# Performance work log

Hardware: AMD Instinct MI355X
Metric: run time of the kernel (lower is better)

Reference implementation:

```python
import jax, jax.numpy as jnp
import numpy as np

V, H, B, T, L, G = 32000, 256, 16, 128, 50, 8
BETA, GAMMA = 5.0, 2.0
ATOL = 1e-8  # torch.allclose(x, zeros) default atol (rtol term vanishes vs zero)


def setup_inputs() -> dict:
    key = jax.random.key(0)
    ks = jax.random.split(key, 17)
    u = 1.0 / np.sqrt(H)
    def U(k, shape):
        return jax.random.uniform(k, shape, jnp.float32, -u, u)
    return dict(
        recipe=jax.random.randint(ks[0], (B, T), 0, V),
        g=jax.random.randint(ks[1], (B, G), 0, V),
        ingr=jax.random.randint(ks[2], (B, L), 0, V),
        wv=jax.random.normal(ks[3], (V, H), jnp.float32) * 0.1,  # frozen word vectors
        w_ih=U(ks[4], (5 * H, H)),
        w_hh=U(ks[5], (5 * H, H)),
        b_ih=U(ks[6], (5 * H,)),
        b_hh=U(ks[7], (5 * H,)),
        Z=U(ks[8], (H, H)),
        Y=U(ks[9], (H, H)),
        U_g=U(ks[10], (H, H)),
        z_bias=U(ks[11], (H,)),
        y_bias=U(ks[12], (H,)),
        S=U(ks[13], (3, H)),
        P=U(ks[14], (H, H)),
        fcW=U(ks[15], (V, H)),
        fcb=U(ks[16], (V,)),
    )


def _cgru_forward(x, g_vec, E, w_ih, w_hh, b_ih, b_hh, Z, Y, U_g, z_bias, y_bias, S, P):
    # x: (B,T,H) batch_first; g_vec: (B,H); E: (B,L,H)
    ht0 = g_vec @ U_g.T                      # init_hidden
    a0 = jnp.zeros((x.shape[0], E.shape[1]), x.dtype)
    E0 = E                                   # (1-a)*E with a=0
    ot0 = jnp.zeros_like(x[:, 0])
    goal_term = g_vec @ Y.T + y_bias         # constant across steps

    def step(carry, x_t):
        ht, ot, a, E_new = carry
        is_zero = jnp.all(jnp.abs(x_t) <= ATOL)
        # --- cell ---
        gi = x_t @ w_ih.T + b_ih
        gh = ht @ w_hh.T + b_hh
        i_r, i_u, i_n, i_g, i_i = jnp.split(gi, 5, axis=1)
        h_r, h_u, h_n, h_g, h_i = jnp.split(gh, 5, axis=1)
        z_t = jax.nn.sigmoid(i_u + h_u)
        r_t = jax.nn.sigmoid(i_r + h_r)
        s_t = jax.nn.sigmoid(i_g + h_g)
        q_t = jax.nn.sigmoid(i_i + h_i)
        tmp = E_new.sum(axis=1)              # 'mlk -> mk'
        h_tilde = jnp.tanh(i_n + r_t * h_n + s_t * goal_term + q_t * (tmp @ Z.T + z_bias))
        ht2 = h_tilde + z_t * (ht - h_tilde)
        # --- attention read/write ---
        ref = jax.nn.softmax((BETA * ht2) @ S.T, axis=-1)   # (B,3)
        h_proj = ht2 @ P.T
        En = (1.0 - a)[:, :, None] * E
        alpha_n = jax.nn.softmax(GAMMA * jnp.einsum('mk,mlk->ml', h_proj, En), axis=-1)
        c_n = jnp.einsum('mlk,ml->mk', E, alpha_n)
        Eu = a[:, :, None] * E
        alpha_u = jax.nn.softmax(GAMMA * jnp.einsum('mk,mlk->ml', h_proj, Eu), axis=-1)
        c_u = jnp.einsum('mlk,ml->mk', E, alpha_u)
        out = ref[:, 0:1] * h_proj + ref[:, 1:2] * c_n + ref[:, 2:3] * c_u
        a2 = a + ref[:, 1:2] * alpha_n
        # skip update when input step is all-zero (faithful to torch.allclose guard)
        ht_o = jnp.where(is_zero, ht, ht2)
        ot_o = jnp.where(is_zero, ot, out)
        a_o = jnp.where(is_zero, a, a2)
        E_o = jnp.where(is_zero, E_new, En)
        return (ht_o, ot_o, a_o, E_o), ot_o

    (ht, ot, a, E_new), outs = jax.lax.scan(step, (ht0, ot0, a0, E0),
                                            jnp.transpose(x, (1, 0, 2)))
    output = jnp.transpose(outs, (1, 0, 2))  # back to batch_first (B,T,H)
    return output, ht, a, E_new


def reference(recipe, g, ingr, wv, w_ih, w_hh, b_ih, b_hh, Z, Y, U_g,
              z_bias, y_bias, S, P, fcW, fcb):
    recipe_embed = wv[recipe]           # (B,T,H)
    goal_embed = wv[g].sum(axis=1)      # (B,H)
    E = wv[ingr]                        # (B,L,H)
    output, ht, a, E_new = _cgru_forward(recipe_embed, goal_embed, E,
                                         w_ih, w_hh, b_ih, b_hh, Z, Y, U_g,
                                         z_bias, y_bias, S, P)
    logits = output @ fcW.T + fcb       # (B,T,V)
    return logits, ht, a, E_new
```

## Files before the change

### kernel.cpp

```cpp
#include <hip/hip_runtime.h>

#define Hd   256
#define Bd   16
#define Td   128
#define Ld   50
#define Vd   32000
#define G5H  1280

typedef __attribute__((ext_vector_type(8))) short short8v;
typedef __attribute__((ext_vector_type(4))) float f32x4;

__device__ __forceinline__ unsigned short f2bu(float f) {
  unsigned u = __float_as_uint(f);
  unsigned r = (u + 0x7fffu + ((u >> 16) & 1u)) >> 16;
  return (unsigned short)r;
}
__device__ __forceinline__ float bu2f(unsigned short b) {
  return __uint_as_float(((unsigned)b) << 16);
}
__device__ __forceinline__ float sigm(float x) { return 1.f / (1.f + __expf(-x)); }

__device__ __forceinline__ void st_devu(unsigned* p, unsigned v) {
  __hip_atomic_store(p, v, __ATOMIC_RELAXED, __HIP_MEMORY_SCOPE_AGENT);
}
__device__ __forceinline__ unsigned ld_devu(const unsigned* p) {
  return __hip_atomic_load((unsigned*)p, __ATOMIC_RELAXED, __HIP_MEMORY_SCOPE_AGENT);
}
__device__ __forceinline__ void st_devd(double* p, double v) {
  __hip_atomic_store(p, v, __ATOMIC_RELAXED, __HIP_MEMORY_SCOPE_AGENT);
}
__device__ __forceinline__ double ld_devd(const double* p) {
  return __hip_atomic_load((double*)p, __ATOMIC_RELAXED, __HIP_MEMORY_SCOPE_AGENT);
}
__device__ __forceinline__ double pk2(float a, float b) {
  union { double d; float2 f; } u; u.f = make_float2(a, b); return u.d;
}

__global__ __launch_bounds__(256) void conv_kernel(
    const float* __restrict__ wv, const float* __restrict__ w_ih,
    const float* __restrict__ fcW, const float* __restrict__ w_hh,
    const float* __restrict__ Zm, const float* __restrict__ Pm,
    unsigned short* __restrict__ wv_b, unsigned short* __restrict__ wih_b,
    unsigned short* __restrict__ fcw_b, unsigned short* __restrict__ whh_f,
    unsigned short* __restrict__ z_f, unsigned short* __restrict__ p_f)
{
  const long N0 = 2048000, N1 = N0 + 81920, N2 = N1 + 2048000;
  const long NW = 81920, NZ = 16384, NP = 16384;
  const long N5 = N2 + NW + NZ + NP;
  for (long idx = (long)blockIdx.x * blockDim.x + threadIdx.x; idx < N5;
       idx += (long)gridDim.x * blockDim.x) {
    if (idx < N2) {
      const float* src; unsigned short* dst; long off;
      if      (idx < N0) { src = wv;   dst = wv_b;  off = idx; }
      else if (idx < N1) { src = w_ih; dst = wih_b; off = idx - N0; }
      else               { src = fcW;  dst = fcw_b; off = idx - N1; }
      float4 v = *(const float4*)(src + off * 4);
      ushort4 o;
      o.x = f2bu(v.x); o.y = f2bu(v.y); o.z = f2bu(v.z); o.w = f2bu(v.w);
      *(ushort4*)(dst + off * 4) = o;
    } else {
      long u = idx - N2;
      const float* src; unsigned short* dst;
      if      (u < NW)      { src = w_hh; dst = whh_f; }
      else if (u < NW + NZ) { src = Zm;   dst = z_f;  u -= NW; }
      else                  { src = Pm;   dst = p_f;  u -= NW + NZ; }
      long frag = u >> 7;
      int g128 = (int)(u & 127);
      int lane = g128 >> 1, e0 = (g128 & 1) * 4;
      long T = frag >> 3; int ks = (int)(frag & 7);
      int lr = lane & 15, lg = lane >> 4;
      float4 v = *(const float4*)(src + (T * 16 + lr) * 256 + ks * 32 + lg * 8 + e0);
      ushort4 o;
      o.x = f2bu(v.x); o.y = f2bu(v.y); o.z = f2bu(v.z); o.w = f2bu(v.w);
      *(ushort4*)(dst + u * 4) = o;
    }
  }
}

__global__ __launch_bounds__(256) void prep_kernel(
    const int* __restrict__ g, const int* __restrict__ ingr,
    const float* __restrict__ wv, const float* __restrict__ Ug,
    const float* __restrict__ Ym, const float* __restrict__ yb,
    float* __restrict__ E_ws, float* __restrict__ sumE,
    float* __restrict__ goal_ws, float* __restrict__ HT0)
{
  __shared__ float ge[256];
  const int b = blockIdx.x, tid = threadIdx.x;
  float s = 0.f;
  for (int i = 0; i < 8; ++i) s += wv[((size_t)g[(b << 3) + i] << 8) + tid];
  ge[tid] = s;
  __syncthreads();
  float h0 = 0.f, gt = 0.f;
  const float* ur = Ug + (tid << 8);
  const float* yr = Ym + (tid << 8);
#pragma unroll 8
  for (int k = 0; k < Hd; k += 4) {
    float4 gv = *(const float4*)(ge + k);
    float4 uv = *(const float4*)(ur + k);
    float4 yv = *(const float4*)(yr + k);
    h0 = fmaf(gv.x, uv.x, h0); h0 = fmaf(gv.y, uv.y, h0);
    h0 = fmaf(gv.z, uv.z, h0); h0 = fmaf(gv.w, uv.w, h0);
    gt = fmaf(gv.x, yv.x, gt); gt = fmaf(gv.y, yv.y, gt);
    gt = fmaf(gv.z, yv.z, gt); gt = fmaf(gv.w, yv.w, gt);
  }
  HT0[(b << 8) + tid] = h0;
  goal_ws[(b << 8) + tid] = gt + yb[tid];
  float se = 0.f;
  for (int l = 0; l < Ld; ++l) {
    float v = wv[((size_t)ingr[b * Ld + l] << 8) + tid];
    E_ws[((size_t)(b * Ld + l) << 8) + tid] = v;
    se += v;
  }
  sumE[(b << 8) + tid] = se;
}

template <int MODE>
__global__ __launch_bounds__(256) void gemm_bf16(
    const unsigned short* __restrict__ A, const unsigned short* __restrict__ Bmat,
    const int* __restrict__ ridx, const float* __restrict__ bias,
    float* __restrict__ C)
{
  __shared__ unsigned short As[128 * 64];
  __shared__ unsigned short Bs[128 * 64];
  const int tid = threadIdx.x;
  const int m0 = blockIdx.x << 7, n0 = blockIdx.y << 7;
  const int wave = tid >> 6, lane = tid & 63;
  const int wm = wave >> 1, wn = wave & 1;
  const int lr = lane & 15, lg = lane >> 4;

  f32x4 acc[4][4];
#pragma unroll
  for (int i = 0; i < 4; ++i)
#pragma unroll
    for (int jj = 0; jj < 4; ++jj) acc[i][jj] = (f32x4){0.f, 0.f, 0.f, 0.f};

  const int srow = tid >> 1, shalf = tid & 1;
  const unsigned short* arow;
  {
    int gm = m0 + srow;
    if (MODE == 0) {
      int tt = gm >> 4, bb = gm & 15;
      arow = A + (size_t)ridx[bb * Td + tt] * Hd;
    } else {
      arow = A + (size_t)gm * Hd;
    }
  }
  const unsigned short* brow = Bmat + (size_t)(n0 + srow) * Hd;

  for (int k0 = 0; k0 < Hd; k0 += 64) {
#pragma unroll
    for (int c = 0; c < 4; ++c) {
      int k = shalf * 32 + c * 8;
      uint4 va = *(const uint4*)(arow + k0 + k);
      uint4 vb = *(const uint4*)(brow + k0 + k);
      int byo = (srow << 7) + ((k << 1) ^ ((srow & 7) << 4));
      *(uint4*)((char*)As + byo) = va;
      *(uint4*)((char*)Bs + byo) = vb;
    }
    __syncthreads();
#pragma unroll
    for (int kk = 0; kk < 2; ++kk) {
      short8v af[4], bfr[4];
      const int kb = kk * 32 + lg * 8;
#pragma unroll
      for (int i = 0; i < 4; ++i) {
        int ar = wm * 64 + i * 16 + lr;
        af[i] = *(const short8v*)((const char*)As + (ar << 7) + ((kb << 1) ^ ((ar & 7) << 4)));
        int br = wn * 64 + i * 16 + lr;
        bfr[i] = *(const short8v*)((const char*)Bs + (br << 7) + ((kb << 1) ^ ((br & 7) << 4)));
      }
#pragma unroll
      for (int i = 0; i < 4; ++i)
#pragma unroll
        for (int jj = 0; jj < 4; ++jj)
          acc[i][jj] = __builtin_amdgcn_mfma_f32_16x16x32_bf16(af[i], bfr[jj], acc[i][jj], 0, 0, 0);
    }
    __syncthreads();
  }
#pragma unroll
  for (int i = 0; i < 4; ++i)
#pragma unroll
    for (int jj = 0; jj < 4; ++jj) {
      int col = n0 + wn * 64 + jj * 16 + lr;
      float bv = bias[col];
#pragma unroll
      for (int r = 0; r < 4; ++r) {
        int row = m0 + wm * 64 + i * 16 + lg * 4 + r;
        float v = acc[i][jj][r] + bv;
        if (MODE == 0) {
          int tt = row >> 4, bb = row & 15;
          C[((size_t)(bb * Td + tt)) * G5H + col] = v;
        } else {
          C[(size_t)row * Vd + col] = v;
        }
      }
    }
}

#define RNN_SMEM 150080
__global__ __launch_bounds__(512, 1) void rnn_kernel(
    const unsigned short* __restrict__ whh_f, const unsigned short* __restrict__ z_f,
    const unsigned short* __restrict__ p_f, const float* __restrict__ b_hh,
    const float* __restrict__ Sm, const float* __restrict__ z_bias,
    const float* __restrict__ gi, const float* __restrict__ goal_ws,
    const float* __restrict__ E_ws, const float* __restrict__ sumE,
    const float* __restrict__ HT0,
    unsigned short* __restrict__ out_all, float* __restrict__ d_out,
    double* __restrict__ XH, double* __restrict__ XP, unsigned* __restrict__ FL)
{
  extern __shared__ char smem[];
  unsigned short* w_lds = (unsigned short*)(smem);
  unsigned short* z_lds = (unsigned short*)(smem + 81920);
  unsigned short* p_lds = (unsigned short*)(smem + 98304);
  unsigned short* E_lds = (unsigned short*)(smem + 114688);
  float* hp    = (float*)(smem + 141088);
  float* gh_l  = (float*)(smem + 142112);
  float* zd    = (float*)(smem + 142752);
  float* se    = (float*)(smem + 142880);
  float* gl    = (float*)(smem + 143904);
  float* bh    = (float*)(smem + 144032);
  float* zb    = (float*)(smem + 144672);
  float* Sl    = (float*)(smem + 144800);
  float* a_l   = (float*)(smem + 145184);
  float* d_l   = (float*)(smem + 145440);
  float* an_l  = (float*)(smem + 145696);
  float* au_l  = (float*)(smem + 145952);
  float* sd    = (float*)(smem + 146208);
  float* refl  = (float*)(smem + 146224);
  unsigned short* tp_hi = (unsigned short*)(smem + 146240);
  unsigned short* tp_lo = (unsigned short*)(smem + 146752);
  unsigned short* hs_hi = (unsigned short*)(smem + 147264);
  unsigned short* hs_lo = (unsigned short*)(smem + 147328);
  float* hrow  = (float*)(smem + 147392);
  unsigned short* ht_hi = (unsigned short*)(smem + 148416);
  unsigned short* ht_lo = (unsigned short*)(smem + 148928);
  float* gi_l  = (float*)(smem + 149440);

  const int b  = blockIdx.x >> 3;
  const int j  = blockIdx.x & 7;
  const int hc0 = j << 5;
  const int tid = threadIdx.x;
  const int lane = tid & 63, wid = tid >> 6;
  const int lr = lane & 15, lg = lane >> 4;
  unsigned* FLb = FL + (b << 5);

  for (int idx = tid; idx < 5120; idx += 512) {
    int f = idx >> 6, e = idx & 63;
    int q = f >> 3, ks = f & 7;
    int T = (q >> 1) * 16 + 2 * j + (q & 1);
    *(uint4*)(w_lds + ((size_t)f << 9) + e * 8) =
        *(const uint4*)(whh_f + (((size_t)T * 8 + ks) << 9) + e * 8);
  }
  for (int idx = tid; idx < 1024; idx += 512) {
    int f = idx >> 6, e = idx & 63;
    int T = 2 * j + (f >> 3), ks = f & 7;
    *(uint4*)(z_lds + ((size_t)f << 9) + e * 8) =
        *(const uint4*)(z_f + (((size_t)T * 8 + ks) << 9) + e * 8);
  }
  for (int idx = tid; idx < 1024; idx += 512) {
    int f = idx >> 6, e = idx & 63;
    *(uint4*)(p_lds + ((size_t)f << 9) + e * 8) =
        *(const uint4*)(p_f + (((size_t)f * 8 + j) << 9) + e * 8);
  }
  for (int idx = tid; idx < Ld * 256; idx += 512) {
    int l = idx >> 8, k = idx & 255;
    E_lds[l * 264 + (k >> 5) * 33 + (k & 31)] =
        f2bu(E_ws[((size_t)(b * Ld + l) << 8) + k]);
  }
  if (tid < 160) bh[tid] = b_hh[((tid >> 5) << 8) + hc0 + (tid & 31)];
  if (tid < 96) Sl[tid] = Sm[((tid >> 5) << 8) + hc0 + (tid & 31)];
  if (tid < 32) {
    gl[tid] = goal_ws[(b << 8) + hc0 + tid];
    zb[tid] = z_bias[hc0 + tid];
  }
  if (tid < 256) {
    float s0 = sumE[(b << 8) + tid];
    se[tid] = s0;
    unsigned short hi = f2bu(s0);
    tp_hi[tid] = hi; tp_lo[tid] = f2bu(s0 - bu2f(hi));
    float h0 = HT0[(b << 8) + tid];
    hrow[tid] = h0;
    unsigned short hh = f2bu(h0);
    ht_hi[tid] = hh; ht_lo[tid] = f2bu(h0 - bu2f(hh));
  }
  if (tid < 64) a_l[tid] = 0.f;
  __syncthreads();

  if (wid < 4) {
#pragma unroll
    for (int i = 0; i < 3; ++i) {
      int q = wid + 4 * i;
      if (q < 10) {
        f32x4 acc = (f32x4){0.f, 0.f, 0.f, 0.f};
#pragma unroll
        for (int ks = 0; ks < 8; ++ks) {
          short8v av = *(const short8v*)(w_lds + ((size_t)(q * 8 + ks) << 9) + (lane << 3));
          short8v bv = (short8v){0,0,0,0,0,0,0,0};
          if (lr < 2)
            bv = *(const short8v*)((lr == 0 ? ht_hi : ht_lo) + ks * 32 + (lg << 3));
          acc = __builtin_amdgcn_mfma_f32_16x16x32_bf16(av, bv, acc, 0, 0, 0);
        }
#pragma unroll
        for (int r = 0; r < 4; ++r) {
          float v = acc[r] + __shfl_xor(acc[r], 1);
          if (lr == 0) gh_l[q * 16 + lg * 4 + r] = v;
        }
      }
    }
  } else if (wid == 4 || wid == 5) {
    int tz = wid - 4;
    f32x4 acc = (f32x4){0.f, 0.f, 0.f, 0.f};
#pragma unroll
    for (int ks = 0; ks < 8; ++ks) {
      short8v av = *(const short8v*)(z_lds + ((size_t)(tz * 8 + ks) << 9) + (lane << 3));
      short8v bv = (short8v){0,0,0,0,0,0,0,0};
      if (lr < 2)
        bv = *(const short8v*)((lr == 0 ? tp_hi : tp_lo) + ks * 32 + (lg << 3));
      acc = __builtin_amdgcn_mfma_f32_16x16x32_bf16(av, bv, acc, 0, 0, 0);
    }
#pragma unroll
    for (int r = 0; r < 4; ++r) {
      float v = acc[r] + __shfl_xor(acc[r], 1);
      if (lr == 0) zd[tz * 16 + lg * 4 + r] = v;
    }
  }
  __syncthreads();
  {
    double* XHp = XH + ((size_t)((0 * 16 + b) * 8 + j)) * 16;
    double* XPp = XP + ((size_t)((0 * 16 + b) * 8 + j)) * 132;
    if (tid < 32) {
      int cl = tid;
      const float* gib = gi + ((size_t)(b * Td)) * G5H + hc0 + cl;
      float g_ir = gib[0], g_iu = gib[256], g_in = gib[512];
      float g_ig = gib[768], g_ii = gib[1024];
      float hr = gh_l[cl]       + bh[cl];
      float hu = gh_l[32 + cl]  + bh[32 + cl];
      float hn = gh_l[64 + cl]  + bh[64 + cl];
      float hg = gh_l[96 + cl]  + bh[96 + cl];
      float hq = gh_l[128 + cl] + bh[128 + cl];
      float rt = sigm(g_ir + hr), zt = sigm(g_iu + hu);
      float st = sigm(g_ig + hg), qt = sigm(g_ii + hq);
      float htl = tanhf(g_in + rt * hn + st * gl[cl] + qt * (zd[cl] + zb[cl]));
      float h2 = htl + zt * (hrow[hc0 + cl] - htl);
      unsigned short hi = f2bu(h2);
      hs_hi[cl] = hi; hs_lo[cl] = f2bu(h2 - bu2f(hi));
      float h2o = __shfl_xor(h2, 1);
      if (!(cl & 1)) st_devd(XHp + (cl >> 1), pk2(h2, h2o));
      float p0 = Sl[cl] * h2, p1 = Sl[32 + cl] * h2, p2 = Sl[64 + cl] * h2;
      p0 += __shfl_xor(p0, 1);  p0 += __shfl_xor(p0, 2);  p0 += __shfl_xor(p0, 4);
      p0 += __shfl_xor(p0, 8);  p0 += __shfl_xor(p0, 16);
      p1 += __shfl_xor(p1, 1);  p1 += __shfl_xor(p1, 2);  p1 += __shfl_xor(p1, 4);
      p1 += __shfl_xor(p1, 8);  p1 += __shfl_xor(p1, 16);
      p2 += __shfl_xor(p2, 1);  p2 += __shfl_xor(p2, 2);  p2 += __shfl_xor(p2, 4);
      p2 += __shfl_xor(p2, 8);  p2 += __shfl_xor(p2, 16);
      if (cl == 0) {
        st_devd(XPp + 128, pk2(p0, p1));
        st_devd(XPp + 129, pk2(p2, 0.f));
      }
    }
    __syncthreads();
#pragma unroll
    for (int qq = 0; qq < 2; ++qq) {
      int q = wid * 2 + qq;
      short8v av = *(const short8v*)(p_lds + ((size_t)q << 9) + (lane << 3));
      short8v bv = (short8v){0,0,0,0,0,0,0,0};
      if (lr < 2)
        bv = *(const short8v*)((lr == 0 ? hs_hi : hs_lo) + (lg << 3));
      f32x4 acc = (f32x4){0.f, 0.f, 0.f, 0.f};
      acc = __builtin_amdgcn_mfma_f32_16x16x32_bf16(av, bv, acc, 0, 0, 0);
      float v0 = acc[0] + __shfl_xor(acc[0], 1);
      float v1 = acc[1] + __shfl_xor(acc[1], 1);
      float v2 = acc[2] + __shfl_xor(acc[2], 1);
      float v3 = acc[3] + __shfl_xor(acc[3], 1);
      if (lr == 0) {
        st_devd(XPp + q * 8 + lg * 2, pk2(v0, v1));
        st_devd(XPp + q * 8 + lg * 2 + 1, pk2(v2, v3));
      }
    }
    asm volatile("s_waitcnt vmcnt(0)" ::: "memory");
    __syncthreads();
    if (tid < 4) st_devu(FLb + j * 4 + tid, 1u);
  }

  for (int t = 0; t < Td; ++t) {
    const int par = t & 1, par1 = (t + 1) & 1;
    const double* XPr = XP + ((size_t)((par * 16 + b) * 8)) * 132;
    const double* XHr = XH + ((size_t)((par * 16 + b) * 8)) * 16;
    double* XPp = XP + ((size_t)((par1 * 16 + b) * 8 + j)) * 132;
    double* XHp = XH + ((size_t)((par1 * 16 + b) * 8 + j)) * 16;
    if (tid < 256) {
      int k = tid;
      int kp = (k >> 5) * 33 + (k & 31);
      float acct = 0.f;
#pragma unroll 10
      for (int l = 0; l < Ld; ++l)
        acct = fmaf(a_l[l], bu2f(E_lds[l * 264 + kp]), acct);
      float tn = se[k] - acct;
      unsigned short th = f2bu(tn);
      tp_hi[k] = th; tp_lo[k] = f2bu(tn - bu2f(th));
    } else {
      unsigned tgt = (unsigned)(t + 1);
      int guard = 0;
      while (1) {
        unsigned v = (lane < 32) ? ld_devu(FLb + lane) : tgt;
        if (__all((int)(v >= tgt))) break;
        __builtin_amdgcn_s_sleep(1);
        if (++guard > (1 << 20)) break;
      }
      int u = tid - 256;
      if (u < 128) {
        float2 f0, f1, f2, f3, f4, f5, f6, f7;
        { union { double d; float2 f; } u_;
          u_.d = ld_devd(XPr + 0 * 132 + u); f0 = u_.f;
          u_.d = ld_devd(XPr + 1 * 132 + u); f1 = u_.f;
          u_.d = ld_devd(XPr + 2 * 132 + u); f2 = u_.f;
          u_.d = ld_devd(XPr + 3 * 132 + u); f3 = u_.f;
          u_.d = ld_devd(XPr + 4 * 132 + u); f4 = u_.f;
          u_.d = ld_devd(XPr + 5 * 132 + u); f5 = u_.f;
          u_.d = ld_devd(XPr + 6 * 132 + u); f6 = u_.f;
          u_.d = ld_devd(XPr + 7 * 132 + u); f7 = u_.f; }
        hp[2 * u] =
          ((((((f0.x + f1.x) + f2.x) + f3.x) + f4.x) + f5.x) + f6.x) + f7.x;
        hp[2 * u + 1] =
          ((((((f0.y + f1.y) + f2.y) + f3.y) + f4.y) + f5.y) + f6.y) + f7.y;
      } else if (u < 192) {
        int d0 = 2 * (u - 128);
#pragma unroll
        for (int s = 0; s < 2; ++s) {
          int d = d0 + s;
          union { double d; float2 f; } u_;
          u_.d = ld_devd(XHr + (d >> 4) * 16 + (d & 15));
          int c0 = (d >> 4) * 32 + 2 * (d & 15);
          float a0 = u_.f.x, a1 = u_.f.y;
          hrow[c0] = a0; hrow[c0 + 1] = a1;
          unsigned short h0 = f2bu(a0), h1 = f2bu(a1);
          ht_hi[c0] = h0;     ht_lo[c0] = f2bu(a0 - bu2f(h0));
          ht_hi[c0 + 1] = h1; ht_lo[c0 + 1] = f2bu(a1 - bu2f(h1));
          if (t == Td - 1 && j == 0) {
            d_out[(size_t)65536000 + (b << 8) + c0] = a0;
            d_out[(size_t)65536000 + (b << 8) + c0 + 1] = a1;
          }
        }
      } else {
        int u2 = u - 192;
        if (u2 < 3) {
          float2 f[8];
#pragma unroll
          for (int js = 0; js < 8; ++js) {
            union { double d; float2 f; } u_;
            u_.d = ld_devd(XPr + js * 132 + 128 + (u2 >> 1));
            f[js] = u_.f;
          }
          float sx, sy;
          sx = ((((((f[0].x + f[1].x) + f[2].x) + f[3].x) + f[4].x) + f[5].x)
                + f[6].x) + f[7].x;
          sy = ((((((f[0].y + f[1].y) + f[2].y) + f[3].y) + f[4].y) + f[5].y)
                + f[6].y) + f[7].y;
          if (u2 == 0) { sd[0] = sx; sd[1] = sy; }
          else if (u2 == 2) sd[2] = sx;
        } else if (u2 >= 8 && u2 < 40 && t < Td - 1) {
          int c = u2 - 8;
          const float* gib = gi + ((size_t)(b * Td + t + 1)) * G5H + hc0 + c;
          gi_l[c]       = gib[0];
          gi_l[32 + c]  = gib[256];
          gi_l[64 + c]  = gib[512];
          gi_l[96 + c]  = gib[768];
          gi_l[128 + c] = gib[1024];
        }
      }
    }
    __syncthreads();
    if (wid < 2) {
      int tz = wid;
      f32x4 acc = (f32x4){0.f, 0.f, 0.f, 0.f};
#pragma unroll
      for (int ks = 0; ks < 8; ++ks) {
        short8v av = *(const short8v*)(z_lds + ((size_t)(tz * 8 + ks) << 9) + (lane << 3));
        short8v bv = (short8v){0,0,0,0,0,0,0,0};
        if (lr < 2)
          bv = *(const short8v*)((lr == 0 ? tp_hi : tp_lo) + ks * 32 + (lg << 3));
        acc = __builtin_amdgcn_mfma_f32_16x16x32_bf16(av, bv, acc, 0, 0, 0);
      }
#pragma unroll
      for (int r = 0; r < 4; ++r) {
        float v = acc[r] + __shfl_xor(acc[r], 1);
        if (lr == 0) zd[tz * 16 + lg * 4 + r] = v;
      }
    } else if (wid < 4) {
#pragma unroll
      for (int i = 0; i < 5; ++i) {
        int q = (wid - 2) * 5 + i;
        f32x4 acc = (f32x4){0.f, 0.f, 0.f, 0.f};
#pragma unroll
        for (int ks = 0; ks < 8; ++ks) {
          short8v av = *(const short8v*)(w_lds + ((size_t)(q * 8 + ks) << 9) + (lane << 3));
          short8v bv = (short8v){0,0,0,0,0,0,0,0};
          if (lr < 2)
            bv = *(const short8v*)((lr == 0 ? ht_hi : ht_lo) + ks * 32 + (lg << 3));
          acc = __builtin_amdgcn_mfma_f32_16x16x32_bf16(av, bv, acc, 0, 0, 0);
        }
#pragma unroll
        for (int r = 0; r < 4; ++r) {
          float v = acc[r] + __shfl_xor(acc[r], 1);
          if (lr == 0) gh_l[q * 16 + lg * 4 + r] = v;
        }
      }
    } else {
      int u = tid - 256;
      if (u < 200) {
        int l = u >> 2, q = u & 3;
        const unsigned short* er0 = E_lds + l * 264 + q * 66;
        const float* hq = hp + (q << 6);
        float p = 0.f;
#pragma unroll 8
        for (int i = 0; i < 16; ++i) {
          unsigned uu = *(const unsigned*)(er0 + 2 * i);
          float e0 = __uint_as_float(uu << 16);
          float e1 = __uint_as_float(uu & 0xffff0000u);
          p = fmaf(e0, hq[2 * i], p);
          p = fmaf(e1, hq[2 * i + 1], p);
        }
        const unsigned short* er1 = er0 + 33;
        const float* hq1 = hq + 32;
#pragma unroll 8
        for (int i = 0; i < 16; ++i) {
          unsigned uu = *(const unsigned*)(er1 + 2 * i);
          float e0 = __uint_as_float(uu << 16);
          float e1 = __uint_as_float(uu & 0xffff0000u);
          p = fmaf(e0, hq1[2 * i], p);
          p = fmaf(e1, hq1[2 * i + 1], p);
        }
        p += __shfl_xor(p, 1); p += __shfl_xor(p, 2);
        if (q == 0) d_l[l] = p;
      } else if (u == 204) {
        float s0 = 5.0f * sd[0], s1 = 5.0f * sd[1], s2 = 5.0f * sd[2];
        float m = fmaxf(s0, fmaxf(s1, s2));
        float e0 = __expf(s0 - m), e1 = __expf(s1 - m), e2 = __expf(s2 - m);
        float inv = 1.f / (e0 + e1 + e2);
        refl[0] = e0 * inv; refl[1] = e1 * inv; refl[2] = e2 * inv;
      }
    }
    __syncthreads();
    if (tid < 32) {
      if (t < Td - 1) {
        int cl = tid;
        float hr = gh_l[cl]       + bh[cl];
        float hu = gh_l[32 + cl]  + bh[32 + cl];
        float hn = gh_l[64 + cl]  + bh[64 + cl];
        float hg = gh_l[96 + cl]  + bh[96 + cl];
        float hq = gh_l[128 + cl] + bh[128 + cl];
        float rt = sigm(gi_l[cl] + hr), zt = sigm(gi_l[32 + cl] + hu);
        float st = sigm(gi_l[96 + cl] + hg), qt = sigm(gi_l[128 + cl] + hq);
        float htl = tanhf(gi_l[64 + cl] + rt * hn + st * gl[cl] + qt * (zd[cl] + zb[cl]));
        float h2 = htl + zt * (hrow[hc0 + cl] - htl);
        unsigned short hi = f2bu(h2);
        hs_hi[cl] = hi; hs_lo[cl] = f2bu(h2 - bu2f(hi));
        float h2o = __shfl_xor(h2, 1);
        if (!(cl & 1)) st_devd(XHp + (cl >> 1), pk2(h2, h2o));
        float p0 = Sl[cl] * h2, p1 = Sl[32 + cl] * h2, p2 = Sl[64 + cl] * h2;
        p0 += __shfl_xor(p0, 1);  p0 += __shfl_xor(p0, 2);  p0 += __shfl_xor(p0, 4);
        p0 += __shfl_xor(p0, 8);  p0 += __shfl_xor(p0, 16);
        p1 += __shfl_xor(p1, 1);  p1 += __shfl_xor(p1, 2);  p1 += __shfl_xor(p1, 4);
        p1 += __shfl_xor(p1, 8);  p1 += __shfl_xor(p1, 16);
        p2 += __shfl_xor(p2, 1);  p2 += __shfl_xor(p2, 2);  p2 += __shfl_xor(p2, 4);
        p2 += __shfl_xor(p2, 8);  p2 += __shfl_xor(p2, 16);
        if (cl == 0) {
          st_devd(XPp + 128, pk2(p0, p1));
          st_devd(XPp + 129, pk2(p2, 0.f));
        }
      }
    } else if (tid >= 64 && tid < 192) {
      int u = tid - 64;
      int which = u >> 6;
      int l = u & 63;
      float dv;
      if (which == 0) dv = (l < Ld) ? 2.0f * (1.f - a_l[l]) * d_l[l] : -3.4e38f;
      else            dv = (l < Ld) ? 2.0f * a_l[l] * d_l[l]         : -3.4e38f;
      float m = dv;
      m = fmaxf(m, __shfl_xor(m, 1));  m = fmaxf(m, __shfl_xor(m, 2));
      m = fmaxf(m, __shfl_xor(m, 4));  m = fmaxf(m, __shfl_xor(m, 8));
      m = fmaxf(m, __shfl_xor(m, 16)); m = fmaxf(m, __shfl_xor(m, 32));
      float e = (l < Ld) ? __expf(dv - m) : 0.f;
      float ss = e;
      ss += __shfl_xor(ss, 1);  ss += __shfl_xor(ss, 2);  ss += __shfl_xor(ss, 4);
      ss += __shfl_xor(ss, 8);  ss += __shfl_xor(ss, 16); ss += __shfl_xor(ss, 32);
      float al = e / ss;
      if (which == 0) an_l[l] = al; else au_l[l] = al;
    }
    __syncthreads();
    if (wid < 4) {
      if (t < Td - 1) {
#pragma unroll
        for (int qq = 0; qq < 4; ++qq) {
          int q = wid * 4 + qq;
          short8v av = *(const short8v*)(p_lds + ((size_t)q << 9) + (lane << 3));
          short8v bv = (short8v){0,0,0,0,0,0,0,0};
          if (lr < 2)
            bv = *(const short8v*)((lr == 0 ? hs_hi : hs_lo) + (lg << 3));
          f32x4 acc = (f32x4){0.f, 0.f, 0.f, 0.f};
          acc = __builtin_amdgcn_mfma_f32_16x16x32_bf16(av, bv, acc, 0, 0, 0);
          float v0 = acc[0] + __shfl_xor(acc[0], 1);
          float v1 = acc[1] + __shfl_xor(acc[1], 1);
          float v2 = acc[2] + __shfl_xor(acc[2], 1);
          float v3 = acc[3] + __shfl_xor(acc[3], 1);
          if (lr == 0) {
            st_devd(XPp + q * 8 + lg * 2, pk2(v0, v1));
            st_devd(XPp + q * 8 + lg * 2 + 1, pk2(v2, v3));
          }
        }
        asm volatile("s_waitcnt vmcnt(0)" ::: "memory");
        if (lane == 0)
          st_devu(FLb + j * 4 + wid, (unsigned)(t + 2));
      }
    } else {
      int k = tid - 256;
      int kp = (k >> 5) * 33 + (k & 31);
      float accn = 0.f, accu = 0.f;
#pragma unroll 10
      for (int l = 0; l < Ld; ++l) {
        float e = bu2f(E_lds[l * 264 + kp]);
        accn = fmaf(an_l[l], e, accn);
        accu = fmaf(au_l[l], e, accu);
      }
      float outv = refl[0] * hp[k] + refl[1] * accn + refl[2] * accu;
      if ((t & 7) == j) {
        out_all[(((b << 7) + t) << 8) + k] = f2bu(outv);
        if (t == Td - 1) {
          for (int l = 0; l < Ld; ++l) {
            size_t o = ((size_t)(b * Ld + l) << 8) + k;
            d_out[(size_t)65540896 + o] = (1.f - a_l[l]) * E_ws[o];
          }
        }
      }
      if (t < Td - 1 && k < Ld)
        a_l[k] = a_l[k] + refl[1] * an_l[k];
    }
    __syncthreads();
    if (t == Td - 1 && tid < Ld) {
      float na = a_l[tid] + refl[1] * an_l[tid];
      if (j == 7) d_out[(size_t)65540096 + b * Ld + tid] = na;
    }
  }
}

extern "C" void kernel_launch(void* const* d_in, const int* in_sizes, int n_in,
                              void* d_out, int out_size, void* d_ws, size_t ws_size,
                              hipStream_t stream)
{
  const int*   recipe = (const int*)d_in[0];
  const int*   g      = (const int*)d_in[1];
  const int*   ingr   = (const int*)d_in[2];
  const float* wv     = (const float*)d_in[3];
  const float* w_ih   = (const float*)d_in[4];
  const float* w_hh   = (const float*)d_in[5];
  const float* b_ih   = (const float*)d_in[6];
  const float* b_hh   = (const float*)d_in[7];
  const float* Z      = (const float*)d_in[8];
  const float* Y      = (const float*)d_in[9];
  const float* Ug     = (const float*)d_in[10];
  const float* z_bias = (const float*)d_in[11];
  const float* y_bias = (const float*)d_in[12];
  const float* S      = (const float*)d_in[13];
  const float* P      = (const float*)d_in[14];
  const float* fcW    = (const float*)d_in[15];
  const float* fcb    = (const float*)d_in[16];
  float* out = (float*)d_out;
  char* ws = (char*)d_ws;

  size_t off = 0;
  unsigned* FL             = (unsigned*)(ws + off);        off += 2048;
  double* XH               = (double*)(ws + off);          off += 32768;
  double* XP               = (double*)(ws + off);          off += 270336;
  unsigned short* wv_b     = (unsigned short*)(ws + off);  off += 16384000;
  unsigned short* wih_b    = (unsigned short*)(ws + off);  off += 655360;
  unsigned short* fcw_b    = (unsigned short*)(ws + off);  off += 16384000;
  unsigned short* whh_f    = (unsigned short*)(ws + off);  off += 655360;
  unsigned short* z_f      = (unsigned short*)(ws + off);  off += 131072;
  unsigned short* p_f      = (unsigned short*)(ws + off);  off += 131072;
  float* gi_ws             = (float*)(ws + off);           off += 10485760;
  float* E_ws              = (float*)(ws + off);           off += 819200;
  float* sumE              = (float*)(ws + off);           off += 16384;
  float* goal_ws           = (float*)(ws + off);           off += 16384;
  float* HT0               = (float*)(ws + off);           off += 16384;
  unsigned short* out_all  = (unsigned short*)(ws + off);  off += 1048576;

  hipMemsetAsync(FL, 0, 2048, stream);
  conv_kernel<<<4096, 256, 0, stream>>>(wv, w_ih, fcW, w_hh, Z, P,
                                        wv_b, wih_b, fcw_b, whh_f, z_f, p_f);
  prep_kernel<<<16, 256, 0, stream>>>(g, ingr, wv, Ug, Y, y_bias,
                                      E_ws, sumE, goal_ws, HT0);
  gemm_bf16<0><<<dim3(16, 10), 256, 0, stream>>>(wv_b, wih_b, recipe, b_ih, gi_ws);
  hipFuncSetAttribute((const void*)rnn_kernel,
                      hipFuncAttributeMaxDynamicSharedMemorySize, RNN_SMEM);
  rnn_kernel<<<128, 512, RNN_SMEM, stream>>>(whh_f, z_f, p_f, b_hh, S, z_bias,
                                             gi_ws, goal_ws, E_ws, sumE, HT0,
                                             out_all, out, XH, XP, FL);
  gemm_bf16<1><<<dim3(16, 250), 256, 0, stream>>>(out_all, fcw_b, nullptr, fcb, out);
}
```

Baseline: 1.354 ms.

## Replace flag-based inter-block barrier with tagged data words in RNN exchange

The per-step cross-block exchange no longer writes payloads, drains the store queue with s_waitcnt, and then publishes a separate flag that consumers poll. Each float value is now packed into a 64-bit atomic store together with a step tag, and consumers poll the data words directly until every tag matches. This removes the store-drain plus flag round trip from the recurrent critical path. In exchange the exchange buffers double in size, more loads are issued while polling, and a larger workspace region must be zeroed before launch.

```diff
diff --git a/kernel.cpp b/kernel.cpp
--- a/kernel.cpp
+++ b/kernel.cpp
@@ -20,12 +20,6 @@
 }
 __device__ __forceinline__ float sigm(float x) { return 1.f / (1.f + __expf(-x)); }
 
-__device__ __forceinline__ void st_devu(unsigned* p, unsigned v) {
-  __hip_atomic_store(p, v, __ATOMIC_RELAXED, __HIP_MEMORY_SCOPE_AGENT);
-}
-__device__ __forceinline__ unsigned ld_devu(const unsigned* p) {
-  return __hip_atomic_load((unsigned*)p, __ATOMIC_RELAXED, __HIP_MEMORY_SCOPE_AGENT);
-}
 __device__ __forceinline__ void st_devd(double* p, double v) {
   __hip_atomic_store(p, v, __ATOMIC_RELAXED, __HIP_MEMORY_SCOPE_AGENT);
 }
@@ -206,7 +200,7 @@
     const float* __restrict__ E_ws, const float* __restrict__ sumE,
     const float* __restrict__ HT0,
     unsigned short* __restrict__ out_all, float* __restrict__ d_out,
-    double* __restrict__ XH, double* __restrict__ XP, unsigned* __restrict__ FL)
+    double* __restrict__ XH, double* __restrict__ XP)
 {
   extern __shared__ char smem[];
   unsigned short* w_lds = (unsigned short*)(smem);
@@ -242,7 +236,6 @@
   const int tid = threadIdx.x;
   const int lane = tid & 63, wid = tid >> 6;
   const int lr = lane & 15, lg = lane >> 4;
-  unsigned* FLb = FL + (b << 5);
 
   for (int idx = tid; idx < 5120; idx += 512) {
     int f = idx >> 6, e = idx & 63;
@@ -326,8 +319,9 @@
   }
   __syncthreads();
   {
-    double* XHp = XH + ((size_t)((0 * 16 + b) * 8 + j)) * 16;
-    double* XPp = XP + ((size_t)((0 * 16 + b) * 8 + j)) * 132;
+    const float tag1 = __uint_as_float(1u);
+    double* XHp = XH + ((size_t)((0 * 16 + b) * 8 + j)) * 32;
+    double* XPp = XP + ((size_t)((0 * 16 + b) * 8 + j)) * 264;
     if (tid < 32) {
       int cl = tid;
       const float* gib = gi + ((size_t)(b * Td)) * G5H + hc0 + cl;
@@ -344,8 +338,7 @@
       float h2 = htl + zt * (hrow[hc0 + cl] - htl);
       unsigned short hi = f2bu(h2);
       hs_hi[cl] = hi; hs_lo[cl] = f2bu(h2 - bu2f(hi));
-      float h2o = __shfl_xor(h2, 1);
-      if (!(cl & 1)) st_devd(XHp + (cl >> 1), pk2(h2, h2o));
+      st_devd(XHp + cl, pk2(h2, tag1));
       float p0 = Sl[cl] * h2, p1 = Sl[32 + cl] * h2, p2 = Sl[64 + cl] * h2;
       p0 += __shfl_xor(p0, 1);  p0 += __shfl_xor(p0, 2);  p0 += __shfl_xor(p0, 4);
       p0 += __shfl_xor(p0, 8);  p0 += __shfl_xor(p0, 16);
@@ -354,8 +347,9 @@
       p2 += __shfl_xor(p2, 1);  p2 += __shfl_xor(p2, 2);  p2 += __shfl_xor(p2, 4);
       p2 += __shfl_xor(p2, 8);  p2 += __shfl_xor(p2, 16);
       if (cl == 0) {
-        st_devd(XPp + 128, pk2(p0, p1));
-        st_devd(XPp + 129, pk2(p2, 0.f));
+        st_devd(XPp + 256, pk2(p0, tag1));
+        st_devd(XPp + 257, pk2(p1, tag1));
+        st_devd(XPp + 258, pk2(p2, tag1));
       }
     }
     __syncthreads();
@@ -368,26 +362,23 @@
         bv = *(const short8v*)((lr == 0 ? hs_hi : hs_lo) + (lg << 3));
       f32x4 acc = (f32x4){0.f, 0.f, 0.f, 0.f};
       acc = __builtin_amdgcn_mfma_f32_16x16x32_bf16(av, bv, acc, 0, 0, 0);
-      float v0 = acc[0] + __shfl_xor(acc[0], 1);
-      float v1 = acc[1] + __shfl_xor(acc[1], 1);
-      float v2 = acc[2] + __shfl_xor(acc[2], 1);
-      float v3 = acc[3] + __shfl_xor(acc[3], 1);
-      if (lr == 0) {
-        st_devd(XPp + q * 8 + lg * 2, pk2(v0, v1));
-        st_devd(XPp + q * 8 + lg * 2 + 1, pk2(v2, v3));
-      }
-    }
-    asm volatile("s_waitcnt vmcnt(0)" ::: "memory");
-    __syncthreads();
-    if (tid < 4) st_devu(FLb + j * 4 + tid, 1u);
-  }
+#pragma unroll
+      for (int r = 0; r < 4; ++r) {
+        float v = acc[r] + __shfl_xor(acc[r], 1);
+        if (lr == 0) st_devd(XPp + q * 16 + lg * 4 + r, pk2(v, tag1));
+      }
+    }
+  }
+  __syncthreads();
 
   for (int t = 0; t < Td; ++t) {
     const int par = t & 1, par1 = (t + 1) & 1;
-    const double* XPr = XP + ((size_t)((par * 16 + b) * 8)) * 132;
-    const double* XHr = XH + ((size_t)((par * 16 + b) * 8)) * 16;
-    double* XPp = XP + ((size_t)((par1 * 16 + b) * 8 + j)) * 132;
-    double* XHp = XH + ((size_t)((par1 * 16 + b) * 8 + j)) * 16;
+    const double* XPr = XP + ((size_t)((par * 16 + b) * 8)) * 264;
+    const double* XHr = XH + ((size_t)((par * 16 + b) * 8)) * 32;
+    double* XPp = XP + ((size_t)((par1 * 16 + b) * 8 + j)) * 264;
+    double* XHp = XH + ((size_t)((par1 * 16 + b) * 8 + j)) * 32;
+    const unsigned tagu = (unsigned)(t + 1);
+    const float tagp = __uint_as_float((unsigned)(t + 2));
     if (tid < 256) {
       int k = tid;
       int kp = (k >> 5) * 33 + (k & 31);
@@ -399,65 +390,95 @@
       unsigned short th = f2bu(tn);
       tp_hi[k] = th; tp_lo[k] = f2bu(tn - bu2f(th));
     } else {
-      unsigned tgt = (unsigned)(t + 1);
-      int guard = 0;
-      while (1) {
-        unsigned v = (lane < 32) ? ld_devu(FLb + lane) : tgt;
-        if (__all((int)(v >= tgt))) break;
-        __builtin_amdgcn_s_sleep(1);
-        if (++guard > (1 << 20)) break;
-      }
       int u = tid - 256;
       if (u < 128) {
-        float2 f0, f1, f2, f3, f4, f5, f6, f7;
-        { union { double d; float2 f; } u_;
-          u_.d = ld_devd(XPr + 0 * 132 + u); f0 = u_.f;
-          u_.d = ld_devd(XPr + 1 * 132 + u); f1 = u_.f;
-          u_.d = ld_devd(XPr + 2 * 132 + u); f2 = u_.f;
-          u_.d = ld_devd(XPr + 3 * 132 + u); f3 = u_.f;
-          u_.d = ld_devd(XPr + 4 * 132 + u); f4 = u_.f;
-          u_.d = ld_devd(XPr + 5 * 132 + u); f5 = u_.f;
-          u_.d = ld_devd(XPr + 6 * 132 + u); f6 = u_.f;
-          u_.d = ld_devd(XPr + 7 * 132 + u); f7 = u_.f; }
-        hp[2 * u] =
-          ((((((f0.x + f1.x) + f2.x) + f3.x) + f4.x) + f5.x) + f6.x) + f7.x;
-        hp[2 * u + 1] =
-          ((((((f0.y + f1.y) + f2.y) + f3.y) + f4.y) + f5.y) + f6.y) + f7.y;
+        int e = 2 * u;
+        float v[16];
+        bool got[16];
+#pragma unroll
+        for (int i = 0; i < 16; ++i) got[i] = false;
+        int guard = 0;
+        while (1) {
+          bool ok = true;
+#pragma unroll
+          for (int js = 0; js < 8; ++js) {
+            if (!got[js]) {
+              union { double d; float2 f; } u_;
+              u_.d = ld_devd(XPr + (size_t)js * 264 + e);
+              if (__float_as_uint(u_.f.y) == tagu) { v[js] = u_.f.x; got[js] = true; }
+              else ok = false;
+            }
+            if (!got[8 + js]) {
+              union { double d; float2 f; } u_;
+              u_.d = ld_devd(XPr + (size_t)js * 264 + e + 1);
+              if (__float_as_uint(u_.f.y) == tagu) { v[8 + js] = u_.f.x; got[8 + js] = true; }
+              else ok = false;
+            }
+          }
+          if (ok) break;
+          __builtin_amdgcn_s_sleep(1);
+          if (++guard > (1 << 20)) break;
+        }
+        hp[e] = ((((((v[0] + v[1]) + v[2]) + v[3]) + v[4]) + v[5]) + v[6]) + v[7];
+        hp[e + 1] =
+          ((((((v[8] + v[9]) + v[10]) + v[11]) + v[12]) + v[13]) + v[14]) + v[15];
       } else if (u < 192) {
-        int d0 = 2 * (u - 128);
-#pragma unroll
-        for (int s = 0; s < 2; ++s) {
-          int d = d0 + s;
-          union { double d; float2 f; } u_;
-          u_.d = ld_devd(XHr + (d >> 4) * 16 + (d & 15));
-          int c0 = (d >> 4) * 32 + 2 * (d & 15);
-          float a0 = u_.f.x, a1 = u_.f.y;
-          hrow[c0] = a0; hrow[c0 + 1] = a1;
-          unsigned short h0 = f2bu(a0), h1 = f2bu(a1);
-          ht_hi[c0] = h0;     ht_lo[c0] = f2bu(a0 - bu2f(h0));
-          ht_hi[c0 + 1] = h1; ht_lo[c0 + 1] = f2bu(a1 - bu2f(h1));
-          if (t == Td - 1 && j == 0) {
-            d_out[(size_t)65536000 + (b << 8) + c0] = a0;
-            d_out[(size_t)65536000 + (b << 8) + c0 + 1] = a1;
+        int c0 = 4 * (u - 128);
+        float h[4];
+        bool got[4];
+#pragma unroll
+        for (int s = 0; s < 4; ++s) got[s] = false;
+        int guard = 0;
+        while (1) {
+          bool ok = true;
+#pragma unroll
+          for (int s = 0; s < 4; ++s) {
+            if (!got[s]) {
+              int c = c0 + s;
+              union { double d; float2 f; } u_;
+              u_.d = ld_devd(XHr + (size_t)(c >> 5) * 32 + (c & 31));
+              if (__float_as_uint(u_.f.y) == tagu) { h[s] = u_.f.x; got[s] = true; }
+              else ok = false;
+            }
           }
+          if (ok) break;
+          __builtin_amdgcn_s_sleep(1);
+          if (++guard > (1 << 20)) break;
+        }
+#pragma unroll
+        for (int s = 0; s < 4; ++s) {
+          int c = c0 + s;
+          hrow[c] = h[s];
+          unsigned short hh = f2bu(h[s]);
+          ht_hi[c] = hh; ht_lo[c] = f2bu(h[s] - bu2f(hh));
+          if (t == Td - 1 && j == 0)
+            d_out[(size_t)65536000 + (b << 8) + c] = h[s];
         }
       } else {
         int u2 = u - 192;
         if (u2 < 3) {
-          float2 f[8];
-#pragma unroll
-          for (int js = 0; js < 8; ++js) {
-            union { double d; float2 f; } u_;
-            u_.d = ld_devd(XPr + js * 132 + 128 + (u2 >> 1));
-            f[js] = u_.f;
+          float sv[8];
+          bool got[8];
+#pragma unroll
+          for (int js = 0; js < 8; ++js) got[js] = false;
+          int guard = 0;
+          while (1) {
+            bool ok = true;
+#pragma unroll
+            for (int js = 0; js < 8; ++js) {
+              if (!got[js]) {
+                union { double d; float2 f; } u_;
+                u_.d = ld_devd(XPr + (size_t)js * 264 + 256 + u2);
+                if (__float_as_uint(u_.f.y) == tagu) { sv[js] = u_.f.x; got[js] = true; }
+                else ok = false;
+              }
+            }
+            if (ok) break;
+            __builtin_amdgcn_s_sleep(1);
+            if (++guard > (1 << 20)) break;
           }
-          float sx, sy;
-          sx = ((((((f[0].x + f[1].x) + f[2].x) + f[3].x) + f[4].x) + f[5].x)
-                + f[6].x) + f[7].x;
-          sy = ((((((f[0].y + f[1].y) + f[2].y) + f[3].y) + f[4].y) + f[5].y)
-                + f[6].y) + f[7].y;
-          if (u2 == 0) { sd[0] = sx; sd[1] = sy; }
-          else if (u2 == 2) sd[2] = sx;
+          sd[u2] =
+            ((((((sv[0] + sv[1]) + sv[2]) + sv[3]) + sv[4]) + sv[5]) + sv[6]) + sv[7];
         } else if (u2 >= 8 && u2 < 40 && t < Td - 1) {
           int c = u2 - 8;
           const float* gib = gi + ((size_t)(b * Td + t + 1)) * G5H + hc0 + c;
@@ -555,8 +576,7 @@
         float h2 = htl + zt * (hrow[hc0 + cl] - htl);
         unsigned short hi = f2bu(h2);
         hs_hi[cl] = hi; hs_lo[cl] = f2bu(h2 - bu2f(hi));
-        float h2o = __shfl_xor(h2, 1);
-        if (!(cl & 1)) st_devd(XHp + (cl >> 1), pk2(h2, h2o));
+        st_devd(XHp + cl, pk2(h2, tagp));
         float p0 = Sl[cl] * h2, p1 = Sl[32 + cl] * h2, p2 = Sl[64 + cl] * h2;
         p0 += __shfl_xor(p0, 1);  p0 += __shfl_xor(p0, 2);  p0 += __shfl_xor(p0, 4);
         p0 += __shfl_xor(p0, 8);  p0 += __shfl_xor(p0, 16);
@@ -565,8 +585,9 @@
         p2 += __shfl_xor(p2, 1);  p2 += __shfl_xor(p2, 2);  p2 += __shfl_xor(p2, 4);
         p2 += __shfl_xor(p2, 8);  p2 += __shfl_xor(p2, 16);
         if (cl == 0) {
-          st_devd(XPp + 128, pk2(p0, p1));
-          st_devd(XPp + 129, pk2(p2, 0.f));
+          st_devd(XPp + 256, pk2(p0, tagp));
+          st_devd(XPp + 257, pk2(p1, tagp));
+          st_devd(XPp + 258, pk2(p2, tagp));
         }
       }
     } else if (tid >= 64 && tid < 192) {
@@ -599,18 +620,12 @@
             bv = *(const short8v*)((lr == 0 ? hs_hi : hs_lo) + (lg << 3));
           f32x4 acc = (f32x4){0.f, 0.f, 0.f, 0.f};
           acc = __builtin_amdgcn_mfma_f32_16x16x32_bf16(av, bv, acc, 0, 0, 0);
-          float v0 = acc[0] + __shfl_xor(acc[0], 1);
-          float v1 = acc[1] + __shfl_xor(acc[1], 1);
-          float v2 = acc[2] + __shfl_xor(acc[2], 1);
-          float v3 = acc[3] + __shfl_xor(acc[3], 1);
-          if (lr == 0) {
-            st_devd(XPp + q * 8 + lg * 2, pk2(v0, v1));
-            st_devd(XPp + q * 8 + lg * 2 + 1, pk2(v2, v3));
+#pragma unroll
+          for (int r = 0; r < 4; ++r) {
+            float v = acc[r] + __shfl_xor(acc[r], 1);
+            if (lr == 0) st_devd(XPp + q * 16 + lg * 4 + r, pk2(v, tagp));
           }
         }
-        asm volatile("s_waitcnt vmcnt(0)" ::: "memory");
-        if (lane == 0)
-          st_devu(FLb + j * 4 + wid, (unsigned)(t + 2));
       }
     } else {
       int k = tid - 256;
@@ -668,9 +683,8 @@
   char* ws = (char*)d_ws;
 
   size_t off = 0;
-  unsigned* FL             = (unsigned*)(ws + off);        off += 2048;
-  double* XH               = (double*)(ws + off);          off += 32768;
-  double* XP               = (double*)(ws + off);          off += 270336;
+  double* XH               = (double*)(ws + off);          off += 65536;
+  double* XP               = (double*)(ws + off);          off += 540672;
   unsigned short* wv_b     = (unsigned short*)(ws + off);  off += 16384000;
   unsigned short* wih_b    = (unsigned short*)(ws + off);  off += 655360;
   unsigned short* fcw_b    = (unsigned short*)(ws + off);  off += 16384000;
@@ -684,7 +698,7 @@
   float* HT0               = (float*)(ws + off);           off += 16384;
   unsigned short* out_all  = (unsigned short*)(ws + off);  off += 1048576;
 
-  hipMemsetAsync(FL, 0, 2048, stream);
+  hipMemsetAsync(XH, 0, 65536 + 540672, stream);
   conv_kernel<<<4096, 256, 0, stream>>>(wv, w_ih, fcW, w_hh, Z, P,
                                         wv_b, wih_b, fcw_b, whh_f, z_f, p_f);
   prep_kernel<<<16, 256, 0, stream>>>(g, ingr, wv, Ug, Y, y_bias,
@@ -694,6 +708,6 @@
                       hipFuncAttributeMaxDynamicSharedMemorySize, RNN_SMEM);
   rnn_kernel<<<128, 512, RNN_SMEM, stream>>>(whh_f, z_f, p_f, b_hh, S, z_bias,
                                              gi_ws, goal_ws, E_ws, sumE, HT0,
-                                             out_all, out, XH, XP, FL);
+                                             out_all, out, XH, XP);
   gemm_bf16<1><<<dim3(16, 250), 256, 0, stream>>>(out_all, fcw_b, nullptr, fcb, out);
 }
```

Result: slower. 1.699 ms (+25.5%).
